# Performance work log

Hardware: AMD Instinct MI355X
Metric: run time of the kernel (lower is better)

Reference implementation:

```python
import jax, jax.numpy as jnp
import numpy as np


def _mirror(idx, n):
    # scipy.ndimage mode='mirror': reflect about edge pixel centers
    # pattern: (d c b | a b c d | c b a), period 2*(n-1)
    p = 2 * (n - 1)
    i = jnp.mod(jnp.abs(idx), p)
    return jnp.where(i >= n, p - i, i)


def _shift_one(img, dydx):
    # img: [H, W]; dydx: [2] -> output[y, x] = img[y - dy, x - dx], bilinear, mirror
    H, W = img.shape
    dy, dx = dydx[0], dydx[1]
    cy = jnp.arange(H, dtype=img.dtype) - dy  # [H] source y coords
    cx = jnp.arange(W, dtype=img.dtype) - dx  # [W] source x coords
    y0f = jnp.floor(cy)
    x0f = jnp.floor(cx)
    fy = cy - y0f  # bilinear fractional weights (differentiable wrt dy)
    fx = cx - x0f
    y0 = y0f.astype(jnp.int32)
    x0 = x0f.astype(jnp.int32)
    y0m = _mirror(y0, H)
    y1m = _mirror(y0 + 1, H)
    x0m = _mirror(x0, W)
    x1m = _mirror(x0 + 1, W)
    # 4-neighbor gathers via outer indexing
    v00 = img[y0m[:, None], x0m[None, :]]
    v01 = img[y0m[:, None], x1m[None, :]]
    v10 = img[y1m[:, None], x0m[None, :]]
    v11 = img[y1m[:, None], x1m[None, :]]
    wy1 = fy[:, None]
    wx1 = fx[None, :]
    return ((1 - wy1) * ((1 - wx1) * v00 + wx1 * v01)
            + wy1 * ((1 - wx1) * v10 + wx1 * v11))


def setup_inputs() -> dict:
    key = jax.random.key(0)
    k1, k2 = jax.random.split(key)
    images = jax.random.normal(k1, (256, 512, 512, 1), dtype=jnp.float32)
    dxdy = jax.random.normal(k2, (256, 2), dtype=jnp.float32)  # trainable 'theta'
    return {"images": images, "dxdy": dxdy}


def reference(images, dxdy):
    imgs = jnp.squeeze(images, -1)  # [N, H, W]
    return jax.vmap(_shift_one)(imgs, dxdy)  # [N, H, W]
```

## Files before the change

### kernel.cpp

```cpp
#include <hip/hip_runtime.h>


typedef float f4u __attribute__((ext_vector_type(4), aligned(4)));

__device__ __forceinline__ int mirror_small(int v) {
    v = abs(v);
    return (v > 511) ? (1022 - v) : v;
}

__global__ __launch_bounds__(256) void shift_bilinear_kernel(
    const float* __restrict__ img,
    const float* __restrict__ dxdy,
    float* __restrict__ out)
{
    constexpr int W = 512, H = 512;

    const int b  = blockIdx.x >> 7;
    const int lp = ((blockIdx.x & 127) << 11) + ((int)threadIdx.x << 3);
    const int y  = lp >> 9;
    const int x8 = lp & (W - 1);

    const float dy = dxdy[2 * b];
    const float dx = dxdy[2 * b + 1];

    const float ny  = -dy,        nx  = -dx;
    const float ayf = floorf(ny), axf = floorf(nx);
    const float fy  = ny - ayf,   fx  = nx - axf;
    const int   ia  = (int)ayf,   ja  = (int)axf;

    const float gy = 1.0f - fy, gx = 1.0f - fx;
    const float w00 = gy * gx, w01 = gy * fx, w10 = fy * gx, w11 = fy * fx;

    const int r0 = mirror_small(y + ia);
    const int r1 = mirror_small(y + ia + 1);
    const float* __restrict__ R0 = img + (b * H + r0) * W;
    const float* __restrict__ R1 = img + (b * H + r1) * W;

    const int xs = x8 + ja;

    float u[9], v[9];
    if (xs >= 0 && xs <= W - 9) {
        const f4u ua = *(const f4u*)(R0 + xs);
        const f4u ub = *(const f4u*)(R0 + xs + 4);
        const f4u va = *(const f4u*)(R1 + xs);
        const f4u vb = *(const f4u*)(R1 + xs + 4);
        u[0]=ua.x; u[1]=ua.y; u[2]=ua.z; u[3]=ua.w;
        u[4]=ub.x; u[5]=ub.y; u[6]=ub.z; u[7]=ub.w; u[8]=R0[xs + 8];
        v[0]=va.x; v[1]=va.y; v[2]=va.z; v[3]=va.w;
        v[4]=vb.x; v[5]=vb.y; v[6]=vb.z; v[7]=vb.w; v[8]=R1[xs + 8];
    } else {
#pragma unroll
        for (int k = 0; k < 9; ++k) {
            const int c = mirror_small(xs + k);
            u[k] = R0[c];
            v[k] = R1[c];
        }
    }

    float4 lo, hi;
    lo.x = w00*u[0] + w01*u[1] + w10*v[0] + w11*v[1];
    lo.y = w00*u[1] + w01*u[2] + w10*v[1] + w11*v[2];
    lo.z = w00*u[2] + w01*u[3] + w10*v[2] + w11*v[3];
    lo.w = w00*u[3] + w01*u[4] + w10*v[3] + w11*v[4];
    hi.x = w00*u[4] + w01*u[5] + w10*v[4] + w11*v[5];
    hi.y = w00*u[5] + w01*u[6] + w10*v[5] + w11*v[6];
    hi.z = w00*u[6] + w01*u[7] + w10*v[6] + w11*v[7];
    hi.w = w00*u[7] + w01*u[8] + w10*v[7] + w11*v[8];

    float* o = out + ((size_t)b << 18) + lp;
    *(float4*)(o)     = lo;
    *(float4*)(o + 4) = hi;
}

extern "C" void kernel_launch(void* const* d_in, const int* in_sizes, int n_in,
                              void* d_out, int out_size, void* d_ws, size_t ws_size,
                              hipStream_t stream) {
    const float* images = (const float*)d_in[0];
    const float* dxdy   = (const float*)d_in[1];
    float*       out    = (float*)d_out;

    const int blocks = out_size >> 11;
    shift_bilinear_kernel<<<blocks, 256, 0, stream>>>(images, dxdy, out);
}
```

Measured before the change: 433.0 us.

## Compute two output rows per thread and share halo column via wave shuffle

Each thread now produces two adjacent output rows, loading three source rows instead of two rows per output row, so the middle row is reused. The ninth column is obtained from the neighbouring lane via __shfl_down rather than a separate scalar load, with lane 63 loading it directly. The grid is halved. This cuts redundant global/L2 reads, but the kernel is likely bandwidth-bound and the cache already served most row reuse, while each thread now holds more registers and there are fewer waves in flight.

```diff
diff --git a/kernel.cpp b/kernel.cpp
--- a/kernel.cpp
+++ b/kernel.cpp
@@ -15,10 +15,12 @@
 {
     constexpr int W = 512, H = 512;
 
-    const int b  = blockIdx.x >> 7;
-    const int lp = ((blockIdx.x & 127) << 11) + ((int)threadIdx.x << 3);
-    const int y  = lp >> 9;
-    const int x8 = lp & (W - 1);
+    const int b    = blockIdx.x >> 6;
+    const int wave = (int)threadIdx.x >> 6;
+    const int lane = (int)threadIdx.x & 63;
+    const int p    = ((blockIdx.x & 63) << 2) + wave;
+    const int y0   = p << 1;
+    const int x8   = lane << 3;
 
     const float dy = dxdy[2 * b];
     const float dx = dxdy[2 * b + 1];
@@ -31,45 +33,75 @@
     const float gy = 1.0f - fy, gx = 1.0f - fx;
     const float w00 = gy * gx, w01 = gy * fx, w10 = fy * gx, w11 = fy * fx;
 
-    const int r0 = mirror_small(y + ia);
-    const int r1 = mirror_small(y + ia + 1);
-    const float* __restrict__ R0 = img + (b * H + r0) * W;
-    const float* __restrict__ R1 = img + (b * H + r1) * W;
+    const int rA = mirror_small(y0 + ia);
+    const int rB = mirror_small(y0 + ia + 1);
+    const int rC = mirror_small(y0 + ia + 2);
+    const float* __restrict__ RA = img + ((size_t)b * H + rA) * W;
+    const float* __restrict__ RB = img + ((size_t)b * H + rB) * W;
+    const float* __restrict__ RC = img + ((size_t)b * H + rC) * W;
 
     const int xs = x8 + ja;
 
-    float u[9], v[9];
-    if (xs >= 0 && xs <= W - 9) {
-        const f4u ua = *(const f4u*)(R0 + xs);
-        const f4u ub = *(const f4u*)(R0 + xs + 4);
-        const f4u va = *(const f4u*)(R1 + xs);
-        const f4u vb = *(const f4u*)(R1 + xs + 4);
-        u[0]=ua.x; u[1]=ua.y; u[2]=ua.z; u[3]=ua.w;
-        u[4]=ub.x; u[5]=ub.y; u[6]=ub.z; u[7]=ub.w; u[8]=R0[xs + 8];
-        v[0]=va.x; v[1]=va.y; v[2]=va.z; v[3]=va.w;
-        v[4]=vb.x; v[5]=vb.y; v[6]=vb.z; v[7]=vb.w; v[8]=R1[xs + 8];
+    float a[8], m[8], c[8];
+    if (xs >= 0 && xs <= W - 8) {
+        const f4u a0 = *(const f4u*)(RA + xs);
+        const f4u a1 = *(const f4u*)(RA + xs + 4);
+        const f4u m0 = *(const f4u*)(RB + xs);
+        const f4u m1 = *(const f4u*)(RB + xs + 4);
+        const f4u c0 = *(const f4u*)(RC + xs);
+        const f4u c1 = *(const f4u*)(RC + xs + 4);
+        a[0]=a0.x; a[1]=a0.y; a[2]=a0.z; a[3]=a0.w;
+        a[4]=a1.x; a[5]=a1.y; a[6]=a1.z; a[7]=a1.w;
+        m[0]=m0.x; m[1]=m0.y; m[2]=m0.z; m[3]=m0.w;
+        m[4]=m1.x; m[5]=m1.y; m[6]=m1.z; m[7]=m1.w;
+        c[0]=c0.x; c[1]=c0.y; c[2]=c0.z; c[3]=c0.w;
+        c[4]=c1.x; c[5]=c1.y; c[6]=c1.z; c[7]=c1.w;
     } else {
 #pragma unroll
-        for (int k = 0; k < 9; ++k) {
-            const int c = mirror_small(xs + k);
-            u[k] = R0[c];
-            v[k] = R1[c];
+        for (int k = 0; k < 8; ++k) {
+            const int col = mirror_small(xs + k);
+            a[k] = RA[col];
+            m[k] = RB[col];
+            c[k] = RC[col];
         }
     }
 
-    float4 lo, hi;
-    lo.x = w00*u[0] + w01*u[1] + w10*v[0] + w11*v[1];
-    lo.y = w00*u[1] + w01*u[2] + w10*v[1] + w11*v[2];
-    lo.z = w00*u[2] + w01*u[3] + w10*v[2] + w11*v[3];
-    lo.w = w00*u[3] + w01*u[4] + w10*v[3] + w11*v[4];
-    hi.x = w00*u[4] + w01*u[5] + w10*v[4] + w11*v[5];
-    hi.y = w00*u[5] + w01*u[6] + w10*v[5] + w11*v[6];
-    hi.z = w00*u[6] + w01*u[7] + w10*v[6] + w11*v[7];
-    hi.w = w00*u[7] + w01*u[8] + w10*v[7] + w11*v[8];
+    float a8 = __shfl_down(a[0], 1);
+    float m8 = __shfl_down(m[0], 1);
+    float c8 = __shfl_down(c[0], 1);
+    if (lane == 63) {
+        const int col = mirror_small(xs + 8);
+        a8 = RA[col];
+        m8 = RB[col];
+        c8 = RC[col];
+    }
 
-    float* o = out + ((size_t)b << 18) + lp;
-    *(float4*)(o)     = lo;
-    *(float4*)(o + 4) = hi;
+    float4 lo0, hi0;
+    lo0.x = w00*a[0] + w01*a[1] + w10*m[0] + w11*m[1];
+    lo0.y = w00*a[1] + w01*a[2] + w10*m[1] + w11*m[2];
+    lo0.z = w00*a[2] + w01*a[3] + w10*m[2] + w11*m[3];
+    lo0.w = w00*a[3] + w01*a[4] + w10*m[3] + w11*m[4];
+    hi0.x = w00*a[4] + w01*a[5] + w10*m[4] + w11*m[5];
+    hi0.y = w00*a[5] + w01*a[6] + w10*m[5] + w11*m[6];
+    hi0.z = w00*a[6] + w01*a[7] + w10*m[6] + w11*m[7];
+    hi0.w = w00*a[7] + w01*a8   + w10*m[7] + w11*m8;
+
+    float4 lo1, hi1;
+    lo1.x = w00*m[0] + w01*m[1] + w10*c[0] + w11*c[1];
+    lo1.y = w00*m[1] + w01*m[2] + w10*c[1] + w11*c[2];
+    lo1.z = w00*m[2] + w01*m[3] + w10*c[2] + w11*c[3];
+    lo1.w = w00*m[3] + w01*m[4] + w10*c[3] + w11*c[4];
+    hi1.x = w00*m[4] + w01*m[5] + w10*c[4] + w11*c[5];
+    hi1.y = w00*m[5] + w01*m[6] + w10*c[5] + w11*c[6];
+    hi1.z = w00*m[6] + w01*m[7] + w10*c[6] + w11*c[7];
+    hi1.w = w00*m[7] + w01*m8   + w10*c[7] + w11*c8;
+
+    float* o0 = out + ((size_t)b << 18) + ((size_t)y0 << 9) + x8;
+    float* o1 = o0 + W;
+    *(float4*)(o0)     = lo0;
+    *(float4*)(o0 + 4) = hi0;
+    *(float4*)(o1)     = lo1;
+    *(float4*)(o1 + 4) = hi1;
 }
 
 extern "C" void kernel_launch(void* const* d_in, const int* in_sizes, int n_in,
@@ -79,6 +111,6 @@
     const float* dxdy   = (const float*)d_in[1];
     float*       out    = (float*)d_out;
 
-    const int blocks = out_size >> 11;
+    const int blocks = out_size >> 12;
     shift_bilinear_kernel<<<blocks, 256, 0, stream>>>(images, dxdy, out);
 }
```

New measurement: 429.7 us. No clear change (-0.8%).
